# Performance work log

Hardware: AMD Instinct MI355X
Metric: run time of the kernel (lower is better)

The kernel has to match this reference:

```python
import jax, jax.numpy as jnp
import numpy as np

EMBED, HEADS, LEVELS, POINTS = 256, 8, 4, 4
SPATIAL_SHAPES = np.array([[128, 128], [64, 64], [32, 32], [16, 16]], dtype=np.int32)


def _grid_init_bias():
    # Faithful reproduction of the sampling_offsets bias init (per-head directional grid).
    thetas = np.arange(HEADS, dtype=np.float32) * (2.0 * np.pi / HEADS)
    g = np.stack([np.cos(thetas), np.sin(thetas)], -1)
    g = g / np.abs(g).max(-1, keepdims=True)
    g = np.tile(g.reshape(HEADS, 1, 1, 2), (1, LEVELS, POINTS, 1))
    for i in range(POINTS):
        g[:, :, i, :] *= i + 1
    return g.reshape(-1).astype(np.float32)


def setup_inputs() -> dict:
    key = jax.random.key(0)
    ks = jax.random.split(key, 8)
    bs = 2
    V = int((SPATIAL_SHAPES[:, 0] * SPATIAL_SHAPES[:, 1]).sum())  # 21760
    Q = V  # encoder self-attention
    C = EMBED
    n_off = HEADS * LEVELS * POINTS * 2
    n_attn = HEADS * LEVELS * POINTS
    inv_sqrt_c = 1.0 / np.sqrt(C)
    return {
        "query": jax.random.normal(ks[0], (bs, Q, C), jnp.float32),
        "value": jax.random.normal(ks[1], (bs, V, C), jnp.float32),
        "reference_points": jax.random.uniform(ks[2], (bs, Q, LEVELS, 2), jnp.float32),
        "spatial_shapes": SPATIAL_SHAPES,  # static int array
        # learned parameters (torch Linear stored as [in, out]: y = x @ W + b)
        "W_off": jax.random.normal(ks[3], (C, n_off), jnp.float32) * 0.01,
        "b_off": jnp.asarray(_grid_init_bias()),
        "W_attn": jax.random.normal(ks[4], (C, n_attn), jnp.float32) * 0.02,
        "b_attn": jnp.zeros((n_attn,), jnp.float32),
        "W_v": jax.random.normal(ks[5], (C, C), jnp.float32) * inv_sqrt_c,
        "b_v": jnp.zeros((C,), jnp.float32),
        "W_out": jax.random.normal(ks[6], (C, C), jnp.float32) * inv_sqrt_c,
        "b_out": jnp.zeros((C,), jnp.float32),
    }


def _ms_deform_attn(query, value, reference_points, shapes,
                    W_off, b_off, W_attn, b_attn, W_v, b_v, W_out, b_out):
    bs, Q, C = query.shape
    d = C // HEADS
    # value projection -> [bs, heads, V, d]
    val = (value @ W_v + b_v).reshape(bs, -1, HEADS, d).transpose(0, 2, 1, 3)
    # sampling offsets and attention weights from query
    off = (query @ W_off + b_off).reshape(bs, Q, HEADS, LEVELS, POINTS, 2)
    attn = jax.nn.softmax(
        (query @ W_attn + b_attn).reshape(bs, Q, HEADS, LEVELS * POINTS), axis=-1
    ).reshape(bs, Q, HEADS, LEVELS, POINTS)
    # offset normalizer is (W, H) per level
    norm = jnp.asarray(np.stack([shapes[:, 1], shapes[:, 0]], -1), jnp.float32)  # [L,2]
    loc = reference_points[:, :, None, :, None, :] + off / norm[None, None, None, :, None, :]

    out = jnp.zeros((bs, HEADS, Q, d), query.dtype)
    start = 0
    for l in range(LEVELS):
        H, W = int(shapes[l, 0]), int(shapes[l, 1])
        v_l = val[:, :, start:start + H * W]  # [bs, heads, H*W, d]
        start += H * W
        loc_l = loc[:, :, :, l]    # [bs, Q, heads, P, 2] in [0,1]
        attn_l = attn[:, :, :, l]  # [bs, Q, heads, P]
        # grid_sample(align_corners=False, padding_mode='zeros') semantics
        g = 2.0 * loc_l - 1.0
        x = (g[..., 0] + 1.0) * 0.5 * W - 0.5
        y = (g[..., 1] + 1.0) * 0.5 * H - 0.5
        x0 = jnp.floor(x)
        y0 = jnp.floor(y)
        for dx in (0, 1):
            for dy in (0, 1):
                xi = x0 + dx
                yi = y0 + dy
                w = (1.0 - jnp.abs(x - xi)) * (1.0 - jnp.abs(y - yi))
                valid = (xi >= 0) & (xi <= W - 1) & (yi >= 0) & (yi <= H - 1)
                w = jnp.where(valid, w, 0.0) * attn_l  # fused corner + attention weight
                idx = (jnp.clip(yi, 0, H - 1).astype(jnp.int32) * W
                       + jnp.clip(xi, 0, W - 1).astype(jnp.int32))  # [bs,Q,heads,P]
                idx_t = jnp.transpose(idx, (0, 2, 1, 3)).reshape(bs, HEADS, Q * POINTS)
                vals = jnp.take_along_axis(v_l, idx_t[..., None], axis=2)
                vals = vals.reshape(bs, HEADS, Q, POINTS, d)
                out = out + jnp.einsum('bhqpd,bqhp->bhqd', vals, w)
    out = out.transpose(0, 2, 1, 3).reshape(bs, Q, C)  # heads-major channel layout
    return out @ W_out + b_out


def reference(query, value, reference_points, spatial_shapes,
              W_off, b_off, W_attn, b_attn, W_v, b_v, W_out, b_out):
    shapes = np.asarray(spatial_shapes)  # static
    return _ms_deform_attn(query, value, reference_points, shapes,
                           W_off, b_off, W_attn, b_attn, W_v, b_v, W_out, b_out)
```

## Files before the change

kernel.cpp:

```cpp
#include <hip/hip_runtime.h>
#include <math.h>

#define QN 21760
#define MTOT 43520

typedef __attribute__((ext_vector_type(8))) short bf16x8;
typedef __attribute__((ext_vector_type(4))) float f32x4;
typedef __attribute__((ext_vector_type(2))) float f32x2;

__device__ inline ushort f2bf(float f) {
  union { float f; uint u; } v; v.f = f;
  return (ushort)((v.u + 0x7FFFu + ((v.u >> 16) & 1u)) >> 16);
}
__device__ inline float bflo(uint u) { union { uint u; float f; } v; v.u = u << 16; return v.f; }
__device__ inline float bfhi(uint u) { union { uint u; float f; } v; v.u = u & 0xFFFF0000u; return v.f; }
__device__ inline uint pk2(float lo, float hi) { return (uint)f2bf(lo) | ((uint)f2bf(hi) << 16); }

__device__ inline void g2l(const ushort* g, ushort* l) {
  __builtin_amdgcn_global_load_lds(
      (const __attribute__((address_space(1))) void*)g,
      (__attribute__((address_space(3))) void*)l, 16, 0, 0);
}

__global__ __launch_bounds__(256) void prep_weights(
    const float* __restrict__ Wv, const float* __restrict__ Wout,
    const float* __restrict__ Woff, const float* __restrict__ Wattn,
    const float* __restrict__ boff, const float* __restrict__ battn,
    ushort* __restrict__ wv_t, ushort* __restrict__ wout_t,
    ushort* __restrict__ wol_t, float* __restrict__ biasf) {
  int bidx = blockIdx.x, t = threadIdx.x;
  if (bidx < 256) {
    int idx = bidx * 256 + t; int n = idx >> 8, k = idx & 255;
    wv_t[idx] = f2bf(Wv[(size_t)k * 256 + n]);
  } else if (bidx < 512) {
    int idx = (bidx - 256) * 256 + t; int n = idx >> 8, k = idx & 255;
    wout_t[idx] = f2bf(Wout[(size_t)k * 256 + n]);
  } else {
    int idx = (bidx - 512) * 256 + t; int n = idx >> 8, k = idx & 255;
    float v = (n < 256) ? Woff[(size_t)k * 256 + n] : Wattn[(size_t)k * 128 + (n - 256)];
    wol_t[idx] = f2bf(v);
    if (idx < 384) biasf[idx] = (idx < 256) ? boff[idx] : battn[idx - 256];
  }
}

__global__ __launch_bounds__(256) void gemm_in(
    const float* __restrict__ value, const float* __restrict__ query,
    const ushort* __restrict__ Wv, const ushort* __restrict__ Wol,
    const float* __restrict__ bv, const float* __restrict__ bol,
    ushort* __restrict__ val_out, float* __restrict__ offlog) {
  __shared__ ushort As[2][4096];
  __shared__ ushort Bs[2][4096];
  const int t = threadIdx.x, wave = t >> 6, lane = t & 63;
  const int bx = blockIdx.x, bm = blockIdx.y * 128;
  const bool isVal = bx < 2;
  const float* A = isVal ? value : query;
  const ushort* Bt = isVal ? (Wv + (size_t)bx * 128 * 256)
                           : (Wol + (size_t)(bx - 2) * 128 * 256);
  const int wm = (wave >> 1) * 64, wn = (wave & 1) * 64;
  const int l15 = lane & 15, l4 = lane >> 4;

  const int srow = lane >> 2, sch = lane & 3;
  const ushort* Bg = Bt + (size_t)(32 * wave + srow) * 256 + sch * 8;
  ushort* lb[2] = { &Bs[0][(32 * wave) * 32], &Bs[1][(32 * wave) * 32] };

  f32x4 acc[4][4];
#pragma unroll
  for (int i = 0; i < 4; ++i)
#pragma unroll
    for (int j = 0; j < 4; ++j) acc[i][j] = (f32x4){0.f, 0.f, 0.f, 0.f};

  {
    float4 pa[4];
#pragma unroll
    for (int i = 0; i < 4; ++i) {
      int c = t + i * 256; int row = c >> 3, part = c & 7;
      pa[i] = *(const float4*)&A[(size_t)(bm + row) * 256 + part * 4];
    }
    g2l(Bg, lb[0]); g2l(Bg + 16 * 256, lb[0] + 16 * 32);
#pragma unroll
    for (int i = 0; i < 4; ++i) {
      int c = t + i * 256; int row = c >> 3, part = c & 7;
      ushort4 hv = { f2bf(pa[i].x), f2bf(pa[i].y), f2bf(pa[i].z), f2bf(pa[i].w) };
      *(ushort4*)&As[0][row * 32 + part * 4] = hv;
    }
  }

  for (int k = 0; k < 8; ++k) {
    __syncthreads();
    const int cur = k & 1, nxt = cur ^ 1;
    float4 pa[4];
    if (k < 7) {
      int k1 = (k + 1) * 32;
#pragma unroll
      for (int i = 0; i < 4; ++i) {
        int c = t + i * 256; int row = c >> 3, part = c & 7;
        pa[i] = *(const float4*)&A[(size_t)(bm + row) * 256 + k1 + part * 4];
      }
      g2l(Bg + k1, lb[nxt]); g2l(Bg + 16 * 256 + k1, lb[nxt] + 16 * 32);
    }
    bf16x8 af[4], bfr[4];
#pragma unroll
    for (int mi = 0; mi < 4; ++mi) af[mi] = *(const bf16x8*)&As[cur][(wm + mi * 16 + l15) * 32 + l4 * 8];
#pragma unroll
    for (int ni = 0; ni < 4; ++ni) bfr[ni] = *(const bf16x8*)&Bs[cur][(wn + ni * 16 + l15) * 32 + l4 * 8];
#pragma unroll
    for (int mi = 0; mi < 4; ++mi)
#pragma unroll
      for (int ni = 0; ni < 4; ++ni)
        acc[mi][ni] = __builtin_amdgcn_mfma_f32_16x16x32_bf16(af[mi], bfr[ni], acc[mi][ni], 0, 0, 0);
    if (k < 7) {
#pragma unroll
      for (int i = 0; i < 4; ++i) {
        int c = t + i * 256; int row = c >> 3, part = c & 7;
        ushort4 hv = { f2bf(pa[i].x), f2bf(pa[i].y), f2bf(pa[i].z), f2bf(pa[i].w) };
        *(ushort4*)&As[nxt][row * 32 + part * 4] = hv;
      }
    }
  }

  if (isVal) {
#pragma unroll
    for (int mi = 0; mi < 4; ++mi)
#pragma unroll
      for (int ni = 0; ni < 4; ++ni) {
        int col = bx * 128 + wn + ni * 16 + l15;
        float bb = bv[col];
        int hh = col >> 5, c = col & 31;
#pragma unroll
        for (int r = 0; r < 4; ++r) {
          int row = bm + wm + mi * 16 + l4 * 4 + r;
          int b = (row >= QN) ? 1 : 0;
          int vpos = row - b * QN;
          val_out[((size_t)(b * 8 + hh) * QN + vpos) * 32 + c] = f2bf(acc[mi][ni][r] + bb);
        }
      }
  } else {
#pragma unroll
    for (int mi = 0; mi < 4; ++mi)
#pragma unroll
      for (int ni = 0; ni < 4; ++ni) {
        int col = (bx - 2) * 128 + wn + ni * 16 + l15;
        float bb = bol[col];
#pragma unroll
        for (int r = 0; r < 4; ++r) {
          int row = bm + wm + mi * 16 + l4 * 4 + r;
          offlog[(size_t)row * 384 + col] = acc[mi][ni][r] + bb;
        }
      }
  }
}

__global__ __launch_bounds__(256) void gemm_out(
    const ushort* __restrict__ A, const ushort* __restrict__ Bt,
    const float* __restrict__ bias, float* __restrict__ C) {
  __shared__ ushort As[2][4096];
  __shared__ ushort Bs[2][4096];
  const int t = threadIdx.x, wave = t >> 6, lane = t & 63;
  const int bm = blockIdx.y * 128, bn = blockIdx.x * 128;
  const int wm = (wave >> 1) * 64, wn = (wave & 1) * 64;
  const int l15 = lane & 15, l4 = lane >> 4;

  const int srow = lane >> 2, sch = lane & 3;
  const ushort* Ag = A + (size_t)(bm + 32 * wave + srow) * 256 + sch * 8;
  const ushort* Bg = Bt + (size_t)(bn + 32 * wave + srow) * 256 + sch * 8;
  ushort* la[2] = { &As[0][(32 * wave) * 32], &As[1][(32 * wave) * 32] };
  ushort* lb[2] = { &Bs[0][(32 * wave) * 32], &Bs[1][(32 * wave) * 32] };

  f32x4 acc[4][4];
#pragma unroll
  for (int i = 0; i < 4; ++i)
#pragma unroll
    for (int j = 0; j < 4; ++j) acc[i][j] = (f32x4){0.f, 0.f, 0.f, 0.f};

  g2l(Ag, la[0]); g2l(Ag + 16 * 256, la[0] + 16 * 32);
  g2l(Bg, lb[0]); g2l(Bg + 16 * 256, lb[0] + 16 * 32);

  for (int k = 0; k < 8; ++k) {
    __syncthreads();
    const int cur = k & 1, nxt = cur ^ 1;
    if (k < 7) {
      int k1 = (k + 1) * 32;
      g2l(Ag + k1, la[nxt]); g2l(Ag + 16 * 256 + k1, la[nxt] + 16 * 32);
      g2l(Bg + k1, lb[nxt]); g2l(Bg + 16 * 256 + k1, lb[nxt] + 16 * 32);
    }
    bf16x8 af[4], bfr[4];
#pragma unroll
    for (int mi = 0; mi < 4; ++mi) af[mi] = *(const bf16x8*)&As[cur][(wm + mi * 16 + l15) * 32 + l4 * 8];
#pragma unroll
    for (int ni = 0; ni < 4; ++ni) bfr[ni] = *(const bf16x8*)&Bs[cur][(wn + ni * 16 + l15) * 32 + l4 * 8];
#pragma unroll
    for (int mi = 0; mi < 4; ++mi)
#pragma unroll
      for (int ni = 0; ni < 4; ++ni)
        acc[mi][ni] = __builtin_amdgcn_mfma_f32_16x16x32_bf16(af[mi], bfr[ni], acc[mi][ni], 0, 0, 0);
  }

#pragma unroll
  for (int mi = 0; mi < 4; ++mi)
#pragma unroll
    for (int ni = 0; ni < 4; ++ni) {
      int col = bn + wn + ni * 16 + l15;
      float bb = bias[col];
#pragma unroll
      for (int r = 0; r < 4; ++r) {
        int row = bm + wm + mi * 16 + l4 * 4 + r;
        C[(size_t)row * 256 + col] = acc[mi][ni][r] + bb;
      }
    }
}

__device__ inline void fma8(f32x2* a, uint4 u, float wv) {
  f32x2 ww = { wv, wv }; f32x2 v;
  v.x = bflo(u.x); v.y = bfhi(u.x); a[0] += v * ww;
  v.x = bflo(u.y); v.y = bfhi(u.y); a[1] += v * ww;
  v.x = bflo(u.z); v.y = bfhi(u.z); a[2] += v * ww;
  v.x = bflo(u.w); v.y = bfhi(u.w); a[3] += v * ww;
}

__global__ __launch_bounds__(256) void msda_sample(
    const ushort* __restrict__ val, const float* __restrict__ offlog,
    const float* __restrict__ ref, ushort* __restrict__ interm) {
  const int lsz[4]    = {128, 64, 32, 16};
  const int lstart[4] = {0, 16384, 20480, 21504};

  int h   = blockIdx.x & 7;
  int z   = blockIdx.x >> 3;
  int sub = threadIdx.x & 1;
  int bq  = z * 128 + (threadIdx.x >> 1);
  int b   = (bq >= QN) ? 1 : 0;

  const float* lgp = offlog + (size_t)bq * 384 + 256 + h * 16;
  float w[16];
  {
    float4 a0 = *(const float4*)(lgp);
    float4 a1 = *(const float4*)(lgp + 4);
    float4 a2 = *(const float4*)(lgp + 8);
    float4 a3 = *(const float4*)(lgp + 12);
    w[0]=a0.x; w[1]=a0.y; w[2]=a0.z; w[3]=a0.w;
    w[4]=a1.x; w[5]=a1.y; w[6]=a1.z; w[7]=a1.w;
    w[8]=a2.x; w[9]=a2.y; w[10]=a2.z; w[11]=a2.w;
    w[12]=a3.x; w[13]=a3.y; w[14]=a3.z; w[15]=a3.w;
  }
  float m = -1e30f;
#pragma unroll
  for (int s = 0; s < 16; ++s) m = fmaxf(m, w[s]);
  float sum = 0.f;
#pragma unroll
  for (int s = 0; s < 16; ++s) { w[s] = __expf(w[s] - m); sum += w[s]; }
  float inv = 1.f / sum;

  const float* offp = offlog + (size_t)bq * 384 + h * 32;
  const float* refp = ref + (size_t)bq * 8;
  const ushort* vb  = val + ((size_t)(b * 8 + h) * QN) * 32 + sub * 16;

  f32x2 acc[8];
#pragma unroll
  for (int i = 0; i < 8; ++i) acc[i] = (f32x2){0.f, 0.f};

#pragma unroll
  for (int l = 0; l < 4; ++l) {
    float4 o0 = *(const float4*)(offp + l * 8);
    float4 o1 = *(const float4*)(offp + l * 8 + 4);
    float ox[4] = { o0.x, o0.z, o1.x, o1.z };
    float oy[4] = { o0.y, o0.w, o1.y, o1.w };
    const int   W = lsz[l];
    const float fW = (float)W;
    const int   base = lstart[l];
    const float rx = refp[l * 2 + 0], ry = refp[l * 2 + 1];
#pragma unroll
    for (int p = 0; p < 4; ++p) {
      float x = rx * fW + ox[p] - 0.5f;
      float y = ry * fW + oy[p] - 0.5f;
      float x0f = floorf(x), y0f = floorf(y);
      int   x0 = (int)x0f,   y0 = (int)y0f;
      float fx = x - x0f,    fy = y - y0f;
      float a = w[l * 4 + p] * inv;
      float wx0 = (x0 >= 0 && x0 < W) ? (1.f - fx) : 0.f;
      float wx1 = (x0 + 1 >= 0 && x0 + 1 < W) ? fx : 0.f;
      float wy0 = (y0 >= 0 && y0 < W) ? (1.f - fy) : 0.f;
      float wy1 = (y0 + 1 >= 0 && y0 + 1 < W) ? fy : 0.f;
      float w00 = wx0 * wy0 * a, w10 = wx1 * wy0 * a;
      float w01 = wx0 * wy1 * a, w11 = wx1 * wy1 * a;

      if (w00 != 0.f) {
        const ushort* pp = vb + (size_t)(base + y0 * W + x0) * 32;
        uint4 u0 = *(const uint4*)pp, u1 = *(const uint4*)(pp + 8);
        fma8(acc, u0, w00); fma8(acc + 4, u1, w00);
      }
      if (w10 != 0.f) {
        const ushort* pp = vb + (size_t)(base + y0 * W + x0 + 1) * 32;
        uint4 u0 = *(const uint4*)pp, u1 = *(const uint4*)(pp + 8);
        fma8(acc, u0, w10); fma8(acc + 4, u1, w10);
      }
      if (w01 != 0.f) {
        const ushort* pp = vb + (size_t)(base + (y0 + 1) * W + x0) * 32;
        uint4 u0 = *(const uint4*)pp, u1 = *(const uint4*)(pp + 8);
        fma8(acc, u0, w01); fma8(acc + 4, u1, w01);
      }
      if (w11 != 0.f) {
        const ushort* pp = vb + (size_t)(base + (y0 + 1) * W + x0 + 1) * 32;
        uint4 u0 = *(const uint4*)pp, u1 = *(const uint4*)(pp + 8);
        fma8(acc, u0, w11); fma8(acc + 4, u1, w11);
      }
    }
  }

  uint4 q0, q1;
  q0.x = pk2(acc[0].x, acc[0].y); q0.y = pk2(acc[1].x, acc[1].y);
  q0.z = pk2(acc[2].x, acc[2].y); q0.w = pk2(acc[3].x, acc[3].y);
  q1.x = pk2(acc[4].x, acc[4].y); q1.y = pk2(acc[5].x, acc[5].y);
  q1.z = pk2(acc[6].x, acc[6].y); q1.w = pk2(acc[7].x, acc[7].y);
  ushort* ip = interm + (size_t)bq * 256 + h * 32 + sub * 16;
  *(uint4*)ip = q0;
  *(uint4*)(ip + 8) = q1;
}

extern "C" void kernel_launch(void* const* d_in, const int* in_sizes, int n_in,
                              void* d_out, int out_size, void* d_ws, size_t ws_size,
                              hipStream_t stream) {
  const float* query = (const float*)d_in[0];
  const float* value = (const float*)d_in[1];
  const float* ref   = (const float*)d_in[2];
  const float* W_off  = (const float*)d_in[4];
  const float* b_off  = (const float*)d_in[5];
  const float* W_attn = (const float*)d_in[6];
  const float* b_attn = (const float*)d_in[7];
  const float* W_v    = (const float*)d_in[8];
  const float* b_v    = (const float*)d_in[9];
  const float* W_out  = (const float*)d_in[10];
  const float* b_out  = (const float*)d_in[11];
  float* out = (float*)d_out;

  char* wsb = (char*)d_ws;
  ushort* ws_wv     = (ushort*)(wsb + 0);
  ushort* ws_wol    = (ushort*)(wsb + 131072);
  ushort* ws_wout   = (ushort*)(wsb + 327680);
  float*  ws_biasf  = (float*)(wsb + 458752);
  ushort* ws_val    = (ushort*)(wsb + 462848);
  ushort* ws_interm = (ushort*)(wsb + 22745088);
  float*  ws_offlog = (float*)(wsb + 45027328);
  size_t need = 45027328 + 66846720;
  if (ws_size < need) return;

  dim3 blk(256);
  prep_weights<<<dim3(896), blk, 0, stream>>>(W_v, W_out, W_off, W_attn, b_off, b_attn,
                                              ws_wv, ws_wout, ws_wol, ws_biasf);
  gemm_in<<<dim3(5, 340), blk, 0, stream>>>(value, query, ws_wv, ws_wol, b_v, ws_biasf,
                                            ws_val, ws_offlog);
  msda_sample<<<dim3(2720), blk, 0, stream>>>(ws_val, ws_offlog, ref, ws_interm);
  gemm_out<<<dim3(2, 340), blk, 0, stream>>>(ws_interm, ws_wout, b_out, out);
}
```

Baseline: 303.7 us.

## Pre-cast inputs to bf16, swizzle GEMM LDS, split sampling across four lanes

Adds a separate kernel that casts query and value to bf16 once. gemm_in then streams A tiles straight into LDS with global_load_lds instead of converting fp32 values in registers, which cuts the fp32 reads repeated across column blocks. Both GEMMs gain an XOR swizzle on LDS chunk positions to reduce bank conflicts. The sampling kernel now uses four threads per query-head, each handling 8 channels, and adds a fast path with unconditional loads of all four corners when they are in bounds. The trade-off is an extra kernel launch, an extra pass over memory for the bf16 copies, and more workspace, with the intermediate buffer now reusing the query-cast region.

```diff
diff --git a/kernel.cpp b/kernel.cpp
--- a/kernel.cpp
+++ b/kernel.cpp
@@ -3,6 +3,7 @@
 
 #define QN 21760
 #define MTOT 43520
+#define SZBQC 11141120
 
 typedef __attribute__((ext_vector_type(8))) short bf16x8;
 typedef __attribute__((ext_vector_type(4))) float f32x4;
@@ -43,8 +44,24 @@
   }
 }
 
+__global__ __launch_bounds__(256) void cast2_bf16(
+    const float* __restrict__ q, const float* __restrict__ v,
+    ushort* __restrict__ qo, ushort* __restrict__ vo) {
+  int i = blockIdx.x * 256 + threadIdx.x;
+  const float* src; ushort* dst;
+  if (i >= SZBQC / 8) { src = q; dst = qo; i -= SZBQC / 8; }
+  else { src = v; dst = vo; }
+  const float4* xp = (const float4*)src;
+  float4 a = xp[2 * i], b = xp[2 * i + 1];
+  uint4 o;
+  o.x = pk2(a.x, a.y); o.y = pk2(a.z, a.w);
+  o.z = pk2(b.x, b.y); o.w = pk2(b.z, b.w);
+  ((uint4*)dst)[i] = o;
+}
+
+
 __global__ __launch_bounds__(256) void gemm_in(
-    const float* __restrict__ value, const float* __restrict__ query,
+    const ushort* __restrict__ vbf, const ushort* __restrict__ qbf,
     const ushort* __restrict__ Wv, const ushort* __restrict__ Wol,
     const float* __restrict__ bv, const float* __restrict__ bol,
     ushort* __restrict__ val_out, float* __restrict__ offlog) {
@@ -53,14 +70,18 @@
   const int t = threadIdx.x, wave = t >> 6, lane = t & 63;
   const int bx = blockIdx.x, bm = blockIdx.y * 128;
   const bool isVal = bx < 2;
-  const float* A = isVal ? value : query;
+  const ushort* A  = isVal ? vbf : qbf;
   const ushort* Bt = isVal ? (Wv + (size_t)bx * 128 * 256)
                            : (Wol + (size_t)(bx - 2) * 128 * 256);
   const int wm = (wave >> 1) * 64, wn = (wave & 1) * 64;
   const int l15 = lane & 15, l4 = lane >> 4;
-
-  const int srow = lane >> 2, sch = lane & 3;
+  const int pc = l4 ^ ((l15 >> 1) & 3);
+
+  const int srow = lane >> 2;
+  const int sch  = (lane & 3) ^ ((lane >> 3) & 3);
+  const ushort* Ag = A + (size_t)(bm + 32 * wave + srow) * 256 + sch * 8;
   const ushort* Bg = Bt + (size_t)(32 * wave + srow) * 256 + sch * 8;
+  ushort* la[2] = { &As[0][(32 * wave) * 32], &As[1][(32 * wave) * 32] };
   ushort* lb[2] = { &Bs[0][(32 * wave) * 32], &Bs[1][(32 * wave) * 32] };
 
   f32x4 acc[4][4];
@@ -69,53 +90,29 @@
 #pragma unroll
     for (int j = 0; j < 4; ++j) acc[i][j] = (f32x4){0.f, 0.f, 0.f, 0.f};
 
-  {
-    float4 pa[4];
-#pragma unroll
-    for (int i = 0; i < 4; ++i) {
-      int c = t + i * 256; int row = c >> 3, part = c & 7;
-      pa[i] = *(const float4*)&A[(size_t)(bm + row) * 256 + part * 4];
-    }
-    g2l(Bg, lb[0]); g2l(Bg + 16 * 256, lb[0] + 16 * 32);
-#pragma unroll
-    for (int i = 0; i < 4; ++i) {
-      int c = t + i * 256; int row = c >> 3, part = c & 7;
-      ushort4 hv = { f2bf(pa[i].x), f2bf(pa[i].y), f2bf(pa[i].z), f2bf(pa[i].w) };
-      *(ushort4*)&As[0][row * 32 + part * 4] = hv;
-    }
-  }
+  g2l(Ag, la[0]); g2l(Ag + 16 * 256, la[0] + 16 * 32);
+  g2l(Bg, lb[0]); g2l(Bg + 16 * 256, lb[0] + 16 * 32);
 
   for (int k = 0; k < 8; ++k) {
     __syncthreads();
     const int cur = k & 1, nxt = cur ^ 1;
-    float4 pa[4];
     if (k < 7) {
       int k1 = (k + 1) * 32;
-#pragma unroll
-      for (int i = 0; i < 4; ++i) {
-        int c = t + i * 256; int row = c >> 3, part = c & 7;
-        pa[i] = *(const float4*)&A[(size_t)(bm + row) * 256 + k1 + part * 4];
-      }
+      g2l(Ag + k1, la[nxt]); g2l(Ag + 16 * 256 + k1, la[nxt] + 16 * 32);
       g2l(Bg + k1, lb[nxt]); g2l(Bg + 16 * 256 + k1, lb[nxt] + 16 * 32);
     }
     bf16x8 af[4], bfr[4];
 #pragma unroll
-    for (int mi = 0; mi < 4; ++mi) af[mi] = *(const bf16x8*)&As[cur][(wm + mi * 16 + l15) * 32 + l4 * 8];
-#pragma unroll
-    for (int ni = 0; ni < 4; ++ni) bfr[ni] = *(const bf16x8*)&Bs[cur][(wn + ni * 16 + l15) * 32 + l4 * 8];
+    for (int mi = 0; mi < 4; ++mi)
+      af[mi] = *(const bf16x8*)&As[cur][(wm + mi * 16 + l15) * 32 + pc * 8];
+#pragma unroll
+    for (int ni = 0; ni < 4; ++ni)
+      bfr[ni] = *(const bf16x8*)&Bs[cur][(wn + ni * 16 + l15) * 32 + pc * 8];
 #pragma unroll
     for (int mi = 0; mi < 4; ++mi)
 #pragma unroll
       for (int ni = 0; ni < 4; ++ni)
         acc[mi][ni] = __builtin_amdgcn_mfma_f32_16x16x32_bf16(af[mi], bfr[ni], acc[mi][ni], 0, 0, 0);
-    if (k < 7) {
-#pragma unroll
-      for (int i = 0; i < 4; ++i) {
-        int c = t + i * 256; int row = c >> 3, part = c & 7;
-        ushort4 hv = { f2bf(pa[i].x), f2bf(pa[i].y), f2bf(pa[i].z), f2bf(pa[i].w) };
-        *(ushort4*)&As[nxt][row * 32 + part * 4] = hv;
-      }
-    }
   }
 
   if (isVal) {
@@ -159,8 +156,10 @@
   const int bm = blockIdx.y * 128, bn = blockIdx.x * 128;
   const int wm = (wave >> 1) * 64, wn = (wave & 1) * 64;
   const int l15 = lane & 15, l4 = lane >> 4;
-
-  const int srow = lane >> 2, sch = lane & 3;
+  const int pc = l4 ^ ((l15 >> 1) & 3);
+
+  const int srow = lane >> 2;
+  const int sch  = (lane & 3) ^ ((lane >> 3) & 3);
   const ushort* Ag = A + (size_t)(bm + 32 * wave + srow) * 256 + sch * 8;
   const ushort* Bg = Bt + (size_t)(bn + 32 * wave + srow) * 256 + sch * 8;
   ushort* la[2] = { &As[0][(32 * wave) * 32], &As[1][(32 * wave) * 32] };
@@ -185,9 +184,11 @@
     }
     bf16x8 af[4], bfr[4];
 #pragma unroll
-    for (int mi = 0; mi < 4; ++mi) af[mi] = *(const bf16x8*)&As[cur][(wm + mi * 16 + l15) * 32 + l4 * 8];
-#pragma unroll
-    for (int ni = 0; ni < 4; ++ni) bfr[ni] = *(const bf16x8*)&Bs[cur][(wn + ni * 16 + l15) * 32 + l4 * 8];
+    for (int mi = 0; mi < 4; ++mi)
+      af[mi] = *(const bf16x8*)&As[cur][(wm + mi * 16 + l15) * 32 + pc * 8];
+#pragma unroll
+    for (int ni = 0; ni < 4; ++ni)
+      bfr[ni] = *(const bf16x8*)&Bs[cur][(wn + ni * 16 + l15) * 32 + pc * 8];
 #pragma unroll
     for (int mi = 0; mi < 4; ++mi)
 #pragma unroll
@@ -225,8 +226,8 @@
 
   int h   = blockIdx.x & 7;
   int z   = blockIdx.x >> 3;
-  int sub = threadIdx.x & 1;
-  int bq  = z * 128 + (threadIdx.x >> 1);
+  int sub = threadIdx.x & 3;
+  int bq  = z * 64 + (threadIdx.x >> 2);
   int b   = (bq >= QN) ? 1 : 0;
 
   const float* lgp = offlog + (size_t)bq * 384 + 256 + h * 16;
@@ -251,11 +252,11 @@
 
   const float* offp = offlog + (size_t)bq * 384 + h * 32;
   const float* refp = ref + (size_t)bq * 8;
-  const ushort* vb  = val + ((size_t)(b * 8 + h) * QN) * 32 + sub * 16;
-
-  f32x2 acc[8];
-#pragma unroll
-  for (int i = 0; i < 8; ++i) acc[i] = (f32x2){0.f, 0.f};
+  const ushort* vb  = val + ((size_t)(b * 8 + h) * QN) * 32 + sub * 8;
+
+  f32x2 acc[4];
+#pragma unroll
+  for (int i = 0; i < 4; ++i) acc[i] = (f32x2){0.f, 0.f};
 
 #pragma unroll
   for (int l = 0; l < 4; ++l) {
@@ -275,44 +276,39 @@
       int   x0 = (int)x0f,   y0 = (int)y0f;
       float fx = x - x0f,    fy = y - y0f;
       float a = w[l * 4 + p] * inv;
-      float wx0 = (x0 >= 0 && x0 < W) ? (1.f - fx) : 0.f;
-      float wx1 = (x0 + 1 >= 0 && x0 + 1 < W) ? fx : 0.f;
-      float wy0 = (y0 >= 0 && y0 < W) ? (1.f - fy) : 0.f;
-      float wy1 = (y0 + 1 >= 0 && y0 + 1 < W) ? fy : 0.f;
-      float w00 = wx0 * wy0 * a, w10 = wx1 * wy0 * a;
-      float w01 = wx0 * wy1 * a, w11 = wx1 * wy1 * a;
-
-      if (w00 != 0.f) {
-        const ushort* pp = vb + (size_t)(base + y0 * W + x0) * 32;
-        uint4 u0 = *(const uint4*)pp, u1 = *(const uint4*)(pp + 8);
-        fma8(acc, u0, w00); fma8(acc + 4, u1, w00);
-      }
-      if (w10 != 0.f) {
-        const ushort* pp = vb + (size_t)(base + y0 * W + x0 + 1) * 32;
-        uint4 u0 = *(const uint4*)pp, u1 = *(const uint4*)(pp + 8);
-        fma8(acc, u0, w10); fma8(acc + 4, u1, w10);
-      }
-      if (w01 != 0.f) {
-        const ushort* pp = vb + (size_t)(base + (y0 + 1) * W + x0) * 32;
-        uint4 u0 = *(const uint4*)pp, u1 = *(const uint4*)(pp + 8);
-        fma8(acc, u0, w01); fma8(acc + 4, u1, w01);
-      }
-      if (w11 != 0.f) {
-        const ushort* pp = vb + (size_t)(base + (y0 + 1) * W + x0 + 1) * 32;
-        uint4 u0 = *(const uint4*)pp, u1 = *(const uint4*)(pp + 8);
-        fma8(acc, u0, w11); fma8(acc + 4, u1, w11);
+      const ushort* r0 = vb + (size_t)(base + y0 * W + x0) * 32;
+      const ushort* r1 = r0 + (size_t)W * 32;
+
+      if (x0 >= 0 && y0 >= 0 && x0 + 1 < W && y0 + 1 < W) {
+        uint4 u00 = *(const uint4*)r0;
+        uint4 u10 = *(const uint4*)(r0 + 32);
+        uint4 u01 = *(const uint4*)r1;
+        uint4 u11 = *(const uint4*)(r1 + 32);
+        float w00 = (1.f - fx) * (1.f - fy) * a;
+        float w10 = fx * (1.f - fy) * a;
+        float w01 = (1.f - fx) * fy * a;
+        float w11 = fx * fy * a;
+        fma8(acc, u00, w00); fma8(acc, u10, w10);
+        fma8(acc, u01, w01); fma8(acc, u11, w11);
+      } else {
+        float wx0 = (x0 >= 0 && x0 < W) ? (1.f - fx) : 0.f;
+        float wx1 = (x0 + 1 >= 0 && x0 + 1 < W) ? fx : 0.f;
+        float wy0 = (y0 >= 0 && y0 < W) ? (1.f - fy) : 0.f;
+        float wy1 = (y0 + 1 >= 0 && y0 + 1 < W) ? fy : 0.f;
+        float w00 = wx0 * wy0 * a, w10 = wx1 * wy0 * a;
+        float w01 = wx0 * wy1 * a, w11 = wx1 * wy1 * a;
+        if (w00 != 0.f) { uint4 u = *(const uint4*)r0;        fma8(acc, u, w00); }
+        if (w10 != 0.f) { uint4 u = *(const uint4*)(r0 + 32); fma8(acc, u, w10); }
+        if (w01 != 0.f) { uint4 u = *(const uint4*)r1;        fma8(acc, u, w01); }
+        if (w11 != 0.f) { uint4 u = *(const uint4*)(r1 + 32); fma8(acc, u, w11); }
       }
     }
   }
 
-  uint4 q0, q1;
-  q0.x = pk2(acc[0].x, acc[0].y); q0.y = pk2(acc[1].x, acc[1].y);
-  q0.z = pk2(acc[2].x, acc[2].y); q0.w = pk2(acc[3].x, acc[3].y);
-  q1.x = pk2(acc[4].x, acc[4].y); q1.y = pk2(acc[5].x, acc[5].y);
-  q1.z = pk2(acc[6].x, acc[6].y); q1.w = pk2(acc[7].x, acc[7].y);
-  ushort* ip = interm + (size_t)bq * 256 + h * 32 + sub * 16;
-  *(uint4*)ip = q0;
-  *(uint4*)(ip + 8) = q1;
+  uint4 o;
+  o.x = pk2(acc[0].x, acc[0].y); o.y = pk2(acc[1].x, acc[1].y);
+  o.z = pk2(acc[2].x, acc[2].y); o.w = pk2(acc[3].x, acc[3].y);
+  *(uint4*)(interm + (size_t)bq * 256 + h * 32 + sub * 8) = o;
 }
 
 extern "C" void kernel_launch(void* const* d_in, const int* in_sizes, int n_in,
@@ -337,16 +333,19 @@
   ushort* ws_wout   = (ushort*)(wsb + 327680);
   float*  ws_biasf  = (float*)(wsb + 458752);
   ushort* ws_val    = (ushort*)(wsb + 462848);
-  ushort* ws_interm = (ushort*)(wsb + 22745088);
-  float*  ws_offlog = (float*)(wsb + 45027328);
-  size_t need = 45027328 + 66846720;
+  ushort* ws_v      = (ushort*)(wsb + 22745088);
+  ushort* ws_q      = (ushort*)(wsb + 45027328);
+  ushort* ws_interm = ws_q;
+  float*  ws_offlog = (float*)(wsb + 67309568);
+  size_t need = (size_t)67309568 + 66846720;
   if (ws_size < need) return;
 
   dim3 blk(256);
   prep_weights<<<dim3(896), blk, 0, stream>>>(W_v, W_out, W_off, W_attn, b_off, b_attn,
                                               ws_wv, ws_wout, ws_wol, ws_biasf);
-  gemm_in<<<dim3(5, 340), blk, 0, stream>>>(value, query, ws_wv, ws_wol, b_v, ws_biasf,
+  cast2_bf16<<<dim3(2 * SZBQC / 8 / 256), blk, 0, stream>>>(query, value, ws_q, ws_v);
+  gemm_in<<<dim3(5, 340), blk, 0, stream>>>(ws_v, ws_q, ws_wv, ws_wol, b_v, ws_biasf,
                                             ws_val, ws_offlog);
-  msda_sample<<<dim3(2720), blk, 0, stream>>>(ws_val, ws_offlog, ref, ws_interm);
+  msda_sample<<<dim3(5440), blk, 0, stream>>>(ws_val, ws_offlog, ref, ws_interm);
   gemm_out<<<dim3(2, 340), blk, 0, stream>>>(ws_interm, ws_wout, b_out, out);
 }
```

Result: no change. 303.4 us (-0.1%).
